# Kernel tuning notes

Hardware: AMD Instinct MI355X
Metric: run time of the kernel (lower is better)

## Reference

```python
import jax, jax.numpy as jnp
import numpy as np
from jax import lax

N = 32768      # n_vertices
E = 512        # embedding_size
D = 32         # padded neighbor-list degree
C = 50         # n_possible_colors (hardcoded in GraphColorizer)
H3 = (E + C) // 2  # 281, fc3 output size


def setup_inputs() -> dict:
    key = jax.random.key(0)
    ks = jax.random.split(key, 10)
    embeddings = jax.random.normal(ks[0], (N, E), dtype=jnp.float32)
    adj = jax.random.randint(ks[1], (N, D), 0, N, dtype=jnp.int32)
    vertex_order = jnp.arange(N, dtype=jnp.int32)  # stand-in for slf_heuristic order
    def lin(k, fi, fo):
        kw, kb = jax.random.split(k)
        s = 1.0 / np.sqrt(fi)
        return (jax.random.uniform(kw, (fi, fo), jnp.float32, -s, s),
                jax.random.uniform(kb, (fo,), jnp.float32, -s, s))
    W1, b1 = lin(ks[2], E, E)
    W2, b2 = lin(ks[3], E, E)
    W3, b3 = lin(ks[4], E, H3)
    W4, b4 = lin(ks[5], H3, C)
    return {"embeddings": embeddings, "adj": adj, "vertex_order": vertex_order,
            "W1": W1, "b1": b1, "W2": W2, "b2": b2,
            "W3": W3, "b3": b3, "W4": W4, "b4": b4}


def reference(embeddings, W1, b1, W2, b2, W3, b3, W4, b4, adj, vertex_order):
    f32 = embeddings.dtype

    def mlp(x):  # ColorClassifier forward (pre-softmax logits)
        h = jax.nn.leaky_relu(x @ W1 + b1)
        h = jax.nn.leaky_relu(h @ W2 + b2)
        h = jax.nn.leaky_relu(h @ W3 + b3)
        return h @ W4 + b4  # [C]

    # on-device categorical sampling via Gumbel-max (replaces np.random.choice)
    gumbel = jax.random.gumbel(jax.random.key(42), (N - 1, C), dtype=jnp.float32)

    # first vertex gets color 0 (self._assign_color(0, vertex_order[0], colors))
    colors0 = jnp.full((N,), -1, dtype=jnp.int32).at[vertex_order[0]].set(0)

    def step(carry, inp):
        colors, logp = carry
        v, g = inp
        ncol = colors[adj[v]]  # colors of neighbors, -1 if unassigned
        # mask adjacent (already used by neighbors) colors; -1 routed to spare slot C
        mask = jnp.zeros((C + 1,), bool).at[jnp.where(ncol >= 0, ncol, C)].set(True)[:C]
        logits = jnp.where(mask, -jnp.inf, mlp(embeddings[v]))
        probs = jax.nn.softmax(logits)
        chosen = jnp.argmax(logits + g)  # ~ categorical(probs)
        colors = colors.at[v].set(chosen.astype(jnp.int32))
        logp = logp + jnp.log(probs[chosen] + 1e-8) - jnp.log(jnp.asarray(1e-8, f32))
        return (colors, logp), None

    (colors, logp), _ = lax.scan(step, (colors0, jnp.asarray(0.0, f32)),
                                 (vertex_order[1:], gumbel))

    confidence = logp / N
    n_used = jnp.sum(jnp.any(colors[:, None] == jnp.arange(C)[None, :], axis=0))
    violation_ratio = jnp.mean((colors[adj] == colors[:, None]).astype(f32))
    cost = n_used.astype(f32) * 1.0 + violation_ratio * 100.0
    reinforce_loss = lax.stop_gradient(cost) * confidence
    return colors, reinforce_loss
```

## Files before the change

### kernel.cpp

```cpp
#include <hip/hip_runtime.h>
#include <cstdint>
#include <cstddef>

#define NV    32768
#define EMB   512
#define DEG   32
#define NC    50
#define H3DIM 281
#define GROWS 32767
#define WGUARD (1u << 20)

__device__ __forceinline__ void threefry(unsigned x0, unsigned x1,
                                         unsigned& y0, unsigned& y1) {
  const unsigned ks0 = 0u, ks1 = 42u, ks2 = 0x1BD11BDAu ^ 42u;
  x0 += ks0; x1 += ks1;
#define TFR(r) { x0 += x1; x1 = (x1 << (r)) | (x1 >> (32 - (r))); x1 ^= x0; }
  TFR(13) TFR(15) TFR(26) TFR(6)  x0 += ks1; x1 += ks2 + 1u;
  TFR(17) TFR(29) TFR(16) TFR(24) x0 += ks2; x1 += ks0 + 2u;
  TFR(13) TFR(15) TFR(26) TFR(6)  x0 += ks0; x1 += ks1 + 3u;
  TFR(17) TFR(29) TFR(16) TFR(24) x0 += ks1; x1 += ks2 + 4u;
  TFR(13) TFR(15) TFR(26) TFR(6)  x0 += ks2; x1 += ks0 + 5u;
#undef TFR
  y0 = x0; y1 = x1;
}

__device__ __forceinline__ float gumbel_at(unsigned idx) {
  unsigned y0, y1;
  threefry(0u, idx, y0, y1);
  unsigned bits = y0 ^ y1;
  unsigned fb = (bits >> 9) | 0x3F800000u;
  float f = __uint_as_float(fb) - 1.0f;
  float u = fmaxf(f, 1.17549435e-38f);
  return -logf(-logf(u));
}

__global__ __launch_bounds__(256) void gemm128(
    const float* __restrict__ A, const float* __restrict__ W,
    const float* __restrict__ bias, float* __restrict__ C,
    int M, int N, int K, int act) {
  __shared__ float As[16][132];
  __shared__ float Bs[16][128];
  int tid = threadIdx.x;
  int bm = blockIdx.y * 128;
  int bn = blockIdx.x * 128;
  int tx = tid & 15, ty = tid >> 4;
  float acc[8][8];
#pragma unroll
  for (int i = 0; i < 8; ++i)
#pragma unroll
    for (int j = 0; j < 8; ++j) acc[i][j] = 0.f;

  for (int k0 = 0; k0 < K; k0 += 16) {
#pragma unroll
    for (int l = 0; l < 2; ++l) {
      int idx = tid + l * 256;
      int row = idx >> 2, cc = (idx & 3) * 4;
      float4 av = *(const float4*)(A + (size_t)(bm + row) * K + (k0 + cc));
      As[cc + 0][row] = av.x; As[cc + 1][row] = av.y;
      As[cc + 2][row] = av.z; As[cc + 3][row] = av.w;
    }
#pragma unroll
    for (int l = 0; l < 2; ++l) {
      int idx = tid + l * 256;
      int row = idx >> 5, cc = (idx & 31) * 4;
      int gc = bn + cc;
      const float* bp = W + (size_t)(k0 + row) * N + gc;
      float4 bv;
      if (gc + 3 < N) bv = *(const float4*)bp;
      else {
        bv.x = (gc + 0 < N) ? bp[0] : 0.f;
        bv.y = (gc + 1 < N) ? bp[1] : 0.f;
        bv.z = (gc + 2 < N) ? bp[2] : 0.f;
        bv.w = (gc + 3 < N) ? bp[3] : 0.f;
      }
      *(float4*)&Bs[row][cc] = bv;
    }
    __syncthreads();
#pragma unroll
    for (int kk = 0; kk < 16; ++kk) {
      float a[8], b[8];
#pragma unroll
      for (int i = 0; i < 8; ++i) a[i] = As[kk][ty * 8 + i];
#pragma unroll
      for (int j = 0; j < 8; ++j) b[j] = Bs[kk][tx * 8 + j];
#pragma unroll
      for (int i = 0; i < 8; ++i)
#pragma unroll
        for (int j = 0; j < 8; ++j)
          acc[i][j] = fmaf(a[i], b[j], acc[i][j]);
    }
    __syncthreads();
  }
#pragma unroll
  for (int i = 0; i < 8; ++i) {
    int row = bm + ty * 8 + i;
#pragma unroll
    for (int j = 0; j < 8; ++j) {
      int cn = bn + tx * 8 + j;
      if (cn < N) {
        float v = acc[i][j] + bias[cn];
        if (act) v = (v >= 0.f) ? v : 0.01f * v;
        C[(size_t)row * N + cn] = v;
      }
    }
  }
}

#define TILE 64
#define BK   16
__global__ __launch_bounds__(256) void gemm_bias_act(
    const float* __restrict__ A, const float* __restrict__ W,
    const float* __restrict__ bias, float* __restrict__ C,
    int M, int N, int K, int act) {
  __shared__ float As[BK][TILE + 1];
  __shared__ float Bs[BK][TILE];
  int tid = threadIdx.x;
  int bm = blockIdx.y * TILE;
  int bn = blockIdx.x * TILE;
  int tx = tid & 15, ty = tid >> 4;
  int ar = tid >> 2;
  int ac = (tid & 3) * 4;
  int br = tid >> 4;
  int bc = (tid & 15) * 4;
  float acc[4][4] = {{0.f,0.f,0.f,0.f},{0.f,0.f,0.f,0.f},{0.f,0.f,0.f,0.f},{0.f,0.f,0.f,0.f}};

  for (int k0 = 0; k0 < K; k0 += BK) {
    {
      int gk = k0 + ac;
      const float* ap = A + (size_t)(bm + ar) * K + gk;
      float a0, a1, a2, a3;
      if (((K & 3) == 0) && (gk + 3 < K)) {
        float4 av = *(const float4*)ap;
        a0 = av.x; a1 = av.y; a2 = av.z; a3 = av.w;
      } else {
        a0 = (gk + 0 < K) ? ap[0] : 0.f;
        a1 = (gk + 1 < K) ? ap[1] : 0.f;
        a2 = (gk + 2 < K) ? ap[2] : 0.f;
        a3 = (gk + 3 < K) ? ap[3] : 0.f;
      }
      As[ac + 0][ar] = a0; As[ac + 1][ar] = a1;
      As[ac + 2][ar] = a2; As[ac + 3][ar] = a3;
    }
    {
      int gr = k0 + br;
      int gc = bn + bc;
      const float* bp = W + (size_t)gr * N + gc;
      float b0 = 0.f, b1 = 0.f, b2 = 0.f, b3 = 0.f;
      if (gr < K) {
        if (((N & 3) == 0) && (gc + 3 < N)) {
          float4 bv = *(const float4*)bp;
          b0 = bv.x; b1 = bv.y; b2 = bv.z; b3 = bv.w;
        } else {
          b0 = (gc + 0 < N) ? bp[0] : 0.f;
          b1 = (gc + 1 < N) ? bp[1] : 0.f;
          b2 = (gc + 2 < N) ? bp[2] : 0.f;
          b3 = (gc + 3 < N) ? bp[3] : 0.f;
        }
      }
      Bs[br][bc + 0] = b0; Bs[br][bc + 1] = b1;
      Bs[br][bc + 2] = b2; Bs[br][bc + 3] = b3;
    }
    __syncthreads();
#pragma unroll
    for (int kk = 0; kk < BK; ++kk) {
      float a[4], b[4];
#pragma unroll
      for (int i = 0; i < 4; ++i) a[i] = As[kk][ty * 4 + i];
#pragma unroll
      for (int j = 0; j < 4; ++j) b[j] = Bs[kk][tx * 4 + j];
#pragma unroll
      for (int i = 0; i < 4; ++i)
#pragma unroll
        for (int j = 0; j < 4; ++j)
          acc[i][j] = fmaf(a[i], b[j], acc[i][j]);
    }
    __syncthreads();
  }
#pragma unroll
  for (int i = 0; i < 4; ++i) {
    int row = bm + ty * 4 + i;
#pragma unroll
    for (int j = 0; j < 4; ++j) {
      int cn = bn + tx * 4 + j;
      if (cn < N) {
        float v = acc[i][j] + bias[cn];
        if (act) v = (v >= 0.f) ? v : 0.01f * v;
        C[(size_t)row * N + cn] = v;
      }
    }
  }
}

__global__ void init_kernel(int* __restrict__ colors,
                            unsigned long long* __restrict__ used,
                            int* __restrict__ icnt) {
  int i = blockIdx.x * 256 + threadIdx.x;
  if (i < NV) colors[i] = -1;
  if (i == 0) { *used = 0ull; icnt[0] = 0; icnt[1] = 0; }
}

__global__ void pos_kernel(const int* __restrict__ order, int* __restrict__ pos) {
  int i = blockIdx.x * 256 + threadIdx.x;
  if (i < NV) pos[order[i]] = i;
}

__global__ void yadd_kernel(const float* __restrict__ logit,
                            const int* __restrict__ order,
                            float* __restrict__ y) {
  int tid = blockIdx.x * 256 + threadIdx.x;
  if (tid >= GROWS * NC) return;
  int p = tid / NC + 1;
  int c = tid - (p - 1) * NC;
  int v = order[p];
  y[p * NC + c] = logit[v * NC + c] + gumbel_at((unsigned)tid);
}

__global__ __launch_bounds__(64) void color_dataflow3(
    const float* __restrict__ y, const int* __restrict__ adj,
    const int* __restrict__ order, const int* __restrict__ pos,
    int* colors, unsigned long long* used) {
  int lane = threadIdx.x;
  int p = blockIdx.x * 64 + lane;
  int v = order[p];
  int u[DEG];
  const int* arow = adj + (size_t)v * DEG;
#pragma unroll
  for (int j = 0; j < DEG; ++j) u[j] = arow[j];
  unsigned pend = 0;
#pragma unroll
  for (int j = 0; j < DEG; ++j)
    if (pos[u[j]] < p) pend |= 1u << j;

  unsigned long long colmask = 0ull;
  unsigned long long um = 0ull;
  bool done = false;
  if (p == 0) {
    __hip_atomic_store(colors + v, 0, __ATOMIC_RELAXED, __HIP_MEMORY_SCOPE_AGENT);
    um = 1ull; done = true; pend = 0;
  }
  unsigned guard = 0;
  while (true) {
    unsigned newpend = pend;
#pragma unroll
    for (int j = 0; j < DEG; ++j) {
      if (pend & (1u << j)) {
        int c = __hip_atomic_load(colors + u[j], __ATOMIC_RELAXED, __HIP_MEMORY_SCOPE_AGENT);
        if (c >= 0) { colmask |= 1ull << c; newpend &= ~(1u << j); }
      }
    }
    pend = newpend;
    if (++guard > WGUARD) pend = 0;
    if (!done && pend == 0) {
      const float* yr = y + (size_t)p * NC;
      float best = -INFINITY;
      int bc = 0;
#pragma unroll
      for (int c = 0; c < NC; ++c) {
        float val = ((colmask >> c) & 1ull) ? -INFINITY : yr[c];
        if (val > best) { best = val; bc = c; }
      }
      __hip_atomic_store(colors + v, bc, __ATOMIC_RELAXED, __HIP_MEMORY_SCOPE_AGENT);
      um |= 1ull << bc;
      done = true;
    }
    if (__ballot(pend != 0) == 0ull) break;
    __builtin_amdgcn_s_sleep(2);
  }
#pragma unroll
  for (int off = 1; off < 64; off <<= 1) um |= __shfl_xor(um, off);
  if (lane == 0) atomicOr(used, um);
}

__global__ __launch_bounds__(256) void logp_kernel(
    const float* __restrict__ logit, const int* __restrict__ adj,
    const int* __restrict__ order, const int* __restrict__ pos,
    const int* __restrict__ colors, float* __restrict__ term) {
  int wid = blockIdx.x * 4 + (threadIdx.x >> 6);
  int lane = threadIdx.x & 63;
  int p = wid + 1;
  if (p >= NV) return;
  int v = order[p];
  int cchosen = colors[v];
  unsigned long long bits = 0ull;
  if (lane < DEG) {
    int u = adj[v * DEG + lane];
    if (pos[u] < p) bits = 1ull << colors[u];
  }
#pragma unroll
  for (int off = 1; off < 64; off <<= 1) bits |= __shfl_xor(bits, off);
  bool masked = (bits >> lane) & 1ull;
  float xv = (lane < NC) ? logit[v * NC + lane] : -INFINITY;
  float x = (lane < NC && !masked) ? xv : -INFINITY;
  float xm = x;
#pragma unroll
  for (int off = 1; off < 64; off <<= 1) xm = fmaxf(xm, __shfl_xor(xm, off));
  float ex = expf(x - xm);
  float S = ex;
#pragma unroll
  for (int off = 1; off < 64; off <<= 1) S += __shfl_xor(S, off);
  float ec = __shfl(ex, cchosen);
  float pr = ec / S;
  if (lane == 0) term[p - 1] = logf(pr + 1e-8f) - logf(1e-8f);
}

__global__ __launch_bounds__(256) void sum_kernel(const float* __restrict__ term,
                                                  float* __restrict__ scal) {
  __shared__ float sm[256];
  float s = 0.f;
  for (int i = threadIdx.x; i < GROWS; i += 256) s += term[i];
  sm[threadIdx.x] = s;
  __syncthreads();
  for (int st = 128; st > 0; st >>= 1) {
    if (threadIdx.x < st) sm[threadIdx.x] += sm[threadIdx.x + st];
    __syncthreads();
  }
  if (threadIdx.x == 0) scal[0] = sm[0];
}

__global__ void violation_kernel(const int* __restrict__ col,
                                 const int* __restrict__ adj,
                                 int* __restrict__ cnt) {
  int idx = blockIdx.x * 256 + threadIdx.x;
  int v = idx >> 5;
  int same = (col[adj[idx]] == col[v]) ? 1 : 0;
  unsigned long long b = __ballot(same);
  if ((threadIdx.x & 63) == 0) atomicAdd(cnt, __popcll(b));
}

__global__ void final_kernel(const int* __restrict__ colors,
                             const float* __restrict__ scal,
                             const unsigned long long* __restrict__ used,
                             const int* __restrict__ icnt,
                             float* __restrict__ out) {
  int i = blockIdx.x * 256 + threadIdx.x;
  if (i < NV) out[i] = (float)colors[i];
  if (i == NV) {
    float logp = scal[0];
    float nused = (float)__popcll(*used);
    float ratio = (float)icnt[1] / 1048576.0f;
    float cost = nused + ratio * 100.0f;
    out[NV] = cost * (logp / 32768.0f);
  }
}

extern "C" void kernel_launch(void* const* d_in, const int* in_sizes, int n_in,
                              void* d_out, int out_size, void* d_ws, size_t ws_size,
                              hipStream_t stream) {
  const float* emb  = (const float*)d_in[0];
  const int*   adj  = (const int*)d_in[1];
  const int*   ord  = (const int*)d_in[2];
  const float* W1   = (const float*)d_in[3];
  const float* b1   = (const float*)d_in[4];
  const float* W2   = (const float*)d_in[5];
  const float* b2   = (const float*)d_in[6];
  const float* W3   = (const float*)d_in[7];
  const float* b3   = (const float*)d_in[8];
  const float* W4   = (const float*)d_in[9];
  const float* b4   = (const float*)d_in[10];
  float* out = (float*)d_out;

  const size_t MB = 1024 * 1024;
  int mt;
  if (ws_size >= 138 * MB)      mt = 32768;
  else if (ws_size >= 51 * MB)  mt = 8192;
  else                          mt = 4096;

  char* ws = (char*)d_ws;
  size_t h1b = (size_t)mt * EMB * 4;
  float* logit = (float*)(ws);
  float* H1t   = (float*)(ws + 7 * MB);
  float* H2t   = (float*)(ws + 7 * MB + h1b);
  float* H3t   = (float*)(ws + 7 * MB + 2 * h1b);
  float* y     = (float*)(ws + 7 * MB);
  char*  sb    = ws + 7 * MB + h1b;
  int*   col32 = (int*)  (sb);
  int*   pos   = (int*)  (sb + 131072);
  float* term  = (float*)(sb + 262144);
  float* scal  = (float*)(sb + 458752);
  unsigned long long* used = (unsigned long long*)(sb + 458752 + 64);
  int*   icnt  = (int*)  (sb + 458752 + 128);

  dim3 blk(256);
  for (int t = 0; t < NV / mt; ++t) {
    const float* embT = emb + (size_t)t * mt * EMB;
    float* logT = logit + (size_t)t * mt * NC;
    gemm128<<<dim3(EMB / 128, mt / 128), blk, 0, stream>>>(
        embT, W1, b1, H1t, mt, EMB, EMB, 1);
    gemm128<<<dim3(EMB / 128, mt / 128), blk, 0, stream>>>(
        H1t, W2, b2, H2t, mt, EMB, EMB, 1);
    gemm128<<<dim3((H3DIM + 127) / 128, mt / 128), blk, 0, stream>>>(
        H2t, W3, b3, H3t, mt, H3DIM, EMB, 1);
    gemm_bias_act<<<dim3(1, mt / TILE), blk, 0, stream>>>(
        H3t, W4, b4, logT, mt, NC, H3DIM, 0);
  }

  init_kernel<<<NV / 256, 256, 0, stream>>>(col32, used, icnt);
  pos_kernel<<<NV / 256, 256, 0, stream>>>(ord, pos);
  yadd_kernel<<<(GROWS * NC + 255) / 256, 256, 0, stream>>>(logit, ord, y);

  color_dataflow3<<<NV / 64, 64, 0, stream>>>(y, adj, ord, pos, col32, used);

  logp_kernel<<<8192, 256, 0, stream>>>(logit, adj, ord, pos, col32, term);
  violation_kernel<<<(NV * DEG) / 256, 256, 0, stream>>>(col32, adj, icnt + 1);
  sum_kernel<<<1, 256, 0, stream>>>(term, scal);

  final_kernel<<<(NV + 1 + 255) / 256, 256, 0, stream>>>(col32, scal, used, icnt, out);
}
```

Measured before the change: 1.467 ms.

## Double-buffer GEMMs, fuse Gumbel into L4 epilogue, pre-rank colors for dataflow

After: 1.763 ms. +20.2%, slower.

```diff
diff --git a/kernel.cpp b/kernel.cpp
--- a/kernel.cpp
+++ b/kernel.cpp
@@ -34,12 +34,12 @@
   return -logf(-logf(u));
 }
 
-__global__ __launch_bounds__(256) void gemm128(
+__global__ __launch_bounds__(256) void gemm128_db(
     const float* __restrict__ A, const float* __restrict__ W,
     const float* __restrict__ bias, float* __restrict__ C,
     int M, int N, int K, int act) {
-  __shared__ float As[16][132];
-  __shared__ float Bs[16][128];
+  __shared__ float As[2][16][132];
+  __shared__ float Bs[2][16][128];
   int tid = threadIdx.x;
   int bm = blockIdx.y * 128;
   int bn = blockIdx.x * 128;
@@ -50,46 +50,68 @@
 #pragma unroll
     for (int j = 0; j < 8; ++j) acc[i][j] = 0.f;
 
-  for (int k0 = 0; k0 < K; k0 += 16) {
+  float4 av[2], bv[2];
+  auto loadA = [&](int k0, int l) {
+    int idx = tid + l * 256;
+    int row = idx >> 2, cc = (idx & 3) * 4;
+    return *(const float4*)(A + (size_t)(bm + row) * K + (k0 + cc));
+  };
+  auto loadB = [&](int k0, int l) {
+    int idx = tid + l * 256;
+    int row = idx >> 5, cc = (idx & 31) * 4;
+    int gc = bn + cc;
+    const float* bp = W + (size_t)(k0 + row) * N + gc;
+    float4 r;
+    if (gc + 3 < N) r = *(const float4*)bp;
+    else {
+      r.x = (gc + 0 < N) ? bp[0] : 0.f;
+      r.y = (gc + 1 < N) ? bp[1] : 0.f;
+      r.z = (gc + 2 < N) ? bp[2] : 0.f;
+      r.w = (gc + 3 < N) ? bp[3] : 0.f;
+    }
+    return r;
+  };
+  auto stash = [&](int buf) {
 #pragma unroll
     for (int l = 0; l < 2; ++l) {
       int idx = tid + l * 256;
       int row = idx >> 2, cc = (idx & 3) * 4;
-      float4 av = *(const float4*)(A + (size_t)(bm + row) * K + (k0 + cc));
-      As[cc + 0][row] = av.x; As[cc + 1][row] = av.y;
-      As[cc + 2][row] = av.z; As[cc + 3][row] = av.w;
-    }
-#pragma unroll
-    for (int l = 0; l < 2; ++l) {
-      int idx = tid + l * 256;
-      int row = idx >> 5, cc = (idx & 31) * 4;
-      int gc = bn + cc;
-      const float* bp = W + (size_t)(k0 + row) * N + gc;
-      float4 bv;
-      if (gc + 3 < N) bv = *(const float4*)bp;
-      else {
-        bv.x = (gc + 0 < N) ? bp[0] : 0.f;
-        bv.y = (gc + 1 < N) ? bp[1] : 0.f;
-        bv.z = (gc + 2 < N) ? bp[2] : 0.f;
-        bv.w = (gc + 3 < N) ? bp[3] : 0.f;
-      }
-      *(float4*)&Bs[row][cc] = bv;
-    }
-    __syncthreads();
+      As[buf][cc + 0][row] = av[l].x; As[buf][cc + 1][row] = av[l].y;
+      As[buf][cc + 2][row] = av[l].z; As[buf][cc + 3][row] = av[l].w;
+      int brow = idx >> 5, bcc = (idx & 31) * 4;
+      *(float4*)&Bs[buf][brow][bcc] = bv[l];
+    }
+  };
+
+  av[0] = loadA(0, 0); av[1] = loadA(0, 1);
+  bv[0] = loadB(0, 0); bv[1] = loadB(0, 1);
+  stash(0);
+  __syncthreads();
+  int T = K >> 4;
+  for (int t = 0; t < T; ++t) {
+    int cur = t & 1;
+    if (t + 1 < T) {
+      int k0 = (t + 1) << 4;
+      av[0] = loadA(k0, 0); av[1] = loadA(k0, 1);
+      bv[0] = loadB(k0, 0); bv[1] = loadB(k0, 1);
+    }
 #pragma unroll
     for (int kk = 0; kk < 16; ++kk) {
       float a[8], b[8];
 #pragma unroll
-      for (int i = 0; i < 8; ++i) a[i] = As[kk][ty * 8 + i];
-#pragma unroll
-      for (int j = 0; j < 8; ++j) b[j] = Bs[kk][tx * 8 + j];
+      for (int i = 0; i < 8; ++i) a[i] = As[cur][kk][ty * 8 + i];
+#pragma unroll
+      for (int j = 0; j < 8; ++j) b[j] = Bs[cur][kk][tx * 8 + j];
 #pragma unroll
       for (int i = 0; i < 8; ++i)
 #pragma unroll
         for (int j = 0; j < 8; ++j)
           acc[i][j] = fmaf(a[i], b[j], acc[i][j]);
     }
-    __syncthreads();
+    if (t + 1 < T) {
+      stash(cur ^ 1);
+      __syncthreads();
+    }
   }
 #pragma unroll
   for (int i = 0; i < 8; ++i) {
@@ -108,15 +130,15 @@
 
 #define TILE 64
 #define BK   16
-__global__ __launch_bounds__(256) void gemm_bias_act(
+__global__ __launch_bounds__(256) void gemm_l4(
     const float* __restrict__ A, const float* __restrict__ W,
-    const float* __restrict__ bias, float* __restrict__ C,
-    int M, int N, int K, int act) {
+    const float* __restrict__ bias, float* __restrict__ Clog,
+    float* __restrict__ y, const int* __restrict__ pos,
+    int row0, int N, int K) {
   __shared__ float As[BK][TILE + 1];
   __shared__ float Bs[BK][TILE];
   int tid = threadIdx.x;
   int bm = blockIdx.y * TILE;
-  int bn = blockIdx.x * TILE;
   int tx = tid & 15, ty = tid >> 4;
   int ar = tid >> 2;
   int ac = (tid & 3) * 4;
@@ -128,37 +150,19 @@
     {
       int gk = k0 + ac;
       const float* ap = A + (size_t)(bm + ar) * K + gk;
-      float a0, a1, a2, a3;
-      if (((K & 3) == 0) && (gk + 3 < K)) {
-        float4 av = *(const float4*)ap;
-        a0 = av.x; a1 = av.y; a2 = av.z; a3 = av.w;
-      } else {
-        a0 = (gk + 0 < K) ? ap[0] : 0.f;
-        a1 = (gk + 1 < K) ? ap[1] : 0.f;
-        a2 = (gk + 2 < K) ? ap[2] : 0.f;
-        a3 = (gk + 3 < K) ? ap[3] : 0.f;
-      }
-      As[ac + 0][ar] = a0; As[ac + 1][ar] = a1;
-      As[ac + 2][ar] = a2; As[ac + 3][ar] = a3;
+      As[ac + 0][ar] = (gk + 0 < K) ? ap[0] : 0.f;
+      As[ac + 1][ar] = (gk + 1 < K) ? ap[1] : 0.f;
+      As[ac + 2][ar] = (gk + 2 < K) ? ap[2] : 0.f;
+      As[ac + 3][ar] = (gk + 3 < K) ? ap[3] : 0.f;
     }
     {
       int gr = k0 + br;
-      int gc = bn + bc;
-      const float* bp = W + (size_t)gr * N + gc;
-      float b0 = 0.f, b1 = 0.f, b2 = 0.f, b3 = 0.f;
-      if (gr < K) {
-        if (((N & 3) == 0) && (gc + 3 < N)) {
-          float4 bv = *(const float4*)bp;
-          b0 = bv.x; b1 = bv.y; b2 = bv.z; b3 = bv.w;
-        } else {
-          b0 = (gc + 0 < N) ? bp[0] : 0.f;
-          b1 = (gc + 1 < N) ? bp[1] : 0.f;
-          b2 = (gc + 2 < N) ? bp[2] : 0.f;
-          b3 = (gc + 3 < N) ? bp[3] : 0.f;
-        }
-      }
-      Bs[br][bc + 0] = b0; Bs[br][bc + 1] = b1;
-      Bs[br][bc + 2] = b2; Bs[br][bc + 3] = b3;
+      const float* bp = W + (size_t)gr * N + bc;
+      bool rok = gr < K;
+      Bs[br][bc + 0] = (rok && bc + 0 < N) ? bp[0] : 0.f;
+      Bs[br][bc + 1] = (rok && bc + 1 < N) ? bp[1] : 0.f;
+      Bs[br][bc + 2] = (rok && bc + 2 < N) ? bp[2] : 0.f;
+      Bs[br][bc + 3] = (rok && bc + 3 < N) ? bp[3] : 0.f;
     }
     __syncthreads();
 #pragma unroll
@@ -178,45 +182,50 @@
   }
 #pragma unroll
   for (int i = 0; i < 4; ++i) {
-    int row = bm + ty * 4 + i;
+    int v = row0 + bm + ty * 4 + i;
+    int p = pos[v];
 #pragma unroll
     for (int j = 0; j < 4; ++j) {
-      int cn = bn + tx * 4 + j;
+      int cn = tx * 4 + j;
       if (cn < N) {
-        float v = acc[i][j] + bias[cn];
-        if (act) v = (v >= 0.f) ? v : 0.01f * v;
-        C[(size_t)row * N + cn] = v;
+        float val = acc[i][j] + bias[cn];
+        Clog[(size_t)v * N + cn] = val;
+        if (p > 0)
+          y[(size_t)p * N + cn] = val + gumbel_at((unsigned)((p - 1) * N + cn));
       }
     }
   }
 }
 
-__global__ void init_kernel(int* __restrict__ colors,
-                            unsigned long long* __restrict__ used,
-                            int* __restrict__ icnt) {
+__global__ void initpos_kernel(const int* __restrict__ order,
+                               int* __restrict__ colors, int* __restrict__ pos,
+                               unsigned long long* __restrict__ used,
+                               int* __restrict__ icnt) {
   int i = blockIdx.x * 256 + threadIdx.x;
-  if (i < NV) colors[i] = -1;
+  if (i < NV) { colors[i] = -1; pos[order[i]] = i; }
   if (i == 0) { *used = 0ull; icnt[0] = 0; icnt[1] = 0; }
 }
 
-__global__ void pos_kernel(const int* __restrict__ order, int* __restrict__ pos) {
-  int i = blockIdx.x * 256 + threadIdx.x;
-  if (i < NV) pos[order[i]] = i;
-}
-
-__global__ void yadd_kernel(const float* __restrict__ logit,
-                            const int* __restrict__ order,
-                            float* __restrict__ y) {
-  int tid = blockIdx.x * 256 + threadIdx.x;
-  if (tid >= GROWS * NC) return;
-  int p = tid / NC + 1;
-  int c = tid - (p - 1) * NC;
-  int v = order[p];
-  y[p * NC + c] = logit[v * NC + c] + gumbel_at((unsigned)tid);
-}
-
-__global__ __launch_bounds__(64) void color_dataflow3(
-    const float* __restrict__ y, const int* __restrict__ adj,
+__global__ __launch_bounds__(256) void rank_kernel(const float* __restrict__ y,
+                                                   unsigned* __restrict__ perm) {
+  __shared__ unsigned char sh[4][64];
+  int w = threadIdx.x >> 6, lane = threadIdx.x & 63;
+  int p = blockIdx.x * 4 + w + 1;
+  bool active = (p < NV);
+  float val = (active && lane < NC) ? y[(size_t)p * NC + lane] : 0.f;
+  int rank = 0;
+#pragma unroll
+  for (int c = 0; c < NC; ++c) {
+    float o = __shfl(val, c);
+    rank += (o > val) || (o == val && c < lane);
+  }
+  if (active && lane < NC) sh[w][rank] = (unsigned char)lane;
+  __syncthreads();
+  if (active && lane < 13) perm[(size_t)p * 13 + lane] = ((unsigned*)sh[w])[lane];
+}
+
+__global__ __launch_bounds__(64) void color_dataflow4(
+    const unsigned* __restrict__ perm, const int* __restrict__ adj,
     const int* __restrict__ order, const int* __restrict__ pos,
     int* colors, unsigned long long* used) {
   int lane = threadIdx.x;
@@ -230,6 +239,9 @@
 #pragma unroll
   for (int j = 0; j < DEG; ++j)
     if (pos[u[j]] < p) pend |= 1u << j;
+  unsigned pm[13];
+#pragma unroll
+  for (int i = 0; i < 13; ++i) pm[i] = perm[(size_t)p * 13 + i];
 
   unsigned long long colmask = 0ull;
   unsigned long long um = 0ull;
@@ -251,13 +263,11 @@
     pend = newpend;
     if (++guard > WGUARD) pend = 0;
     if (!done && pend == 0) {
-      const float* yr = y + (size_t)p * NC;
-      float best = -INFINITY;
-      int bc = 0;
-#pragma unroll
-      for (int c = 0; c < NC; ++c) {
-        float val = ((colmask >> c) & 1ull) ? -INFINITY : yr[c];
-        if (val > best) { best = val; bc = c; }
+      int bc = -1;
+#pragma unroll
+      for (int r = 0; r < NC; ++r) {
+        int c = (int)((pm[r >> 2] >> ((r & 3) * 8)) & 0xffu);
+        if (bc < 0 && !((colmask >> c) & 1ull)) bc = c;
       }
       __hip_atomic_store(colors + v, bc, __ATOMIC_RELAXED, __HIP_MEMORY_SCOPE_AGENT);
       um |= 1ull << bc;
@@ -361,44 +371,43 @@
 
   const size_t MB = 1024 * 1024;
   int mt;
-  if (ws_size >= 138 * MB)      mt = 32768;
-  else if (ws_size >= 51 * MB)  mt = 8192;
+  if (ws_size >= 175 * MB)      mt = 32768;
+  else if (ws_size >= 52 * MB)  mt = 8192;
   else                          mt = 4096;
 
   char* ws = (char*)d_ws;
+  int*   col32 = (int*)  (ws);
+  int*   pos   = (int*)  (ws + 131072);
+  float* term  = (float*)(ws + 262144);
+  float* scal  = (float*)(ws + 393216);
+  unsigned long long* used = (unsigned long long*)(ws + 393216 + 64);
+  int*   icnt  = (int*)  (ws + 393216 + 128);
+  unsigned* perm = (unsigned*)(ws + 512 * 1024);
+  float* logit = (float*)(ws + 3 * MB);
   size_t h1b = (size_t)mt * EMB * 4;
-  float* logit = (float*)(ws);
-  float* H1t   = (float*)(ws + 7 * MB);
-  float* H2t   = (float*)(ws + 7 * MB + h1b);
-  float* H3t   = (float*)(ws + 7 * MB + 2 * h1b);
-  float* y     = (float*)(ws + 7 * MB);
-  char*  sb    = ws + 7 * MB + h1b;
-  int*   col32 = (int*)  (sb);
-  int*   pos   = (int*)  (sb + 131072);
-  float* term  = (float*)(sb + 262144);
-  float* scal  = (float*)(sb + 458752);
-  unsigned long long* used = (unsigned long long*)(sb + 458752 + 64);
-  int*   icnt  = (int*)  (sb + 458752 + 128);
+  float* H1t   = (float*)(ws + 10 * MB);
+  float* H2t   = (float*)(ws + 10 * MB + h1b);
+  float* H3t   = (float*)(ws + 10 * MB + 2 * h1b);
+  float* y     = (float*)(ws + 10 * MB);
 
   dim3 blk(256);
+  initpos_kernel<<<NV / 256, 256, 0, stream>>>(ord, col32, pos, used, icnt);
+
   for (int t = 0; t < NV / mt; ++t) {
     const float* embT = emb + (size_t)t * mt * EMB;
-    float* logT = logit + (size_t)t * mt * NC;
-    gemm128<<<dim3(EMB / 128, mt / 128), blk, 0, stream>>>(
+    gemm128_db<<<dim3(EMB / 128, mt / 128), blk, 0, stream>>>(
         embT, W1, b1, H1t, mt, EMB, EMB, 1);
-    gemm128<<<dim3(EMB / 128, mt / 128), blk, 0, stream>>>(
+    gemm128_db<<<dim3(EMB / 128, mt / 128), blk, 0, stream>>>(
         H1t, W2, b2, H2t, mt, EMB, EMB, 1);
-    gemm128<<<dim3((H3DIM + 127) / 128, mt / 128), blk, 0, stream>>>(
+    gemm128_db<<<dim3((H3DIM + 127) / 128, mt / 128), blk, 0, stream>>>(
         H2t, W3, b3, H3t, mt, H3DIM, EMB, 1);
-    gemm_bias_act<<<dim3(1, mt / TILE), blk, 0, stream>>>(
-        H3t, W4, b4, logT, mt, NC, H3DIM, 0);
-  }
-
-  init_kernel<<<NV / 256, 256, 0, stream>>>(col32, used, icnt);
-  pos_kernel<<<NV / 256, 256, 0, stream>>>(ord, pos);
-  yadd_kernel<<<(GROWS * NC + 255) / 256, 256, 0, stream>>>(logit, ord, y);
-
-  color_dataflow3<<<NV / 64, 64, 0, stream>>>(y, adj, ord, pos, col32, used);
+    gemm_l4<<<dim3(1, mt / TILE), blk, 0, stream>>>(
+        H3t, W4, b4, logit, y, pos, t * mt, NC, H3DIM);
+  }
+
+  rank_kernel<<<(GROWS + 3) / 4, 256, 0, stream>>>(y, perm);
+
+  color_dataflow4<<<NV / 64, 64, 0, stream>>>(perm, adj, ord, pos, col32, used);
 
   logp_kernel<<<8192, 256, 0, stream>>>(logit, adj, ord, pos, col32, term);
   violation_kernel<<<(NV * DEG) / 256, 256, 0, stream>>>(col32, adj, icnt + 1);
```
